# Kernel tuning notes

Hardware: AMD Instinct MI355X
Metric: run time of the kernel (lower is better)

Reference implementation:

```python
import jax, jax.numpy as jnp
import numpy as np

H = 16        # num_attention_heads
D = 1024      # hidden_size
HD = D // H   # attention_head_size = 64

def setup_inputs() -> dict:
    key = jax.random.key(0)
    ks = jax.random.split(key, 5)
    scale = 0.02
    return {
        "hidden_states": jax.random.normal(ks[0], (4, 2048, D), dtype=jnp.float32),
        "attention_mask": jnp.zeros((4, 2048), dtype=jnp.float32),
        "Wq": jax.random.normal(ks[1], (D, D), dtype=jnp.float32) * scale,
        "bq": jnp.zeros((D,), dtype=jnp.float32),
        "Wk": jax.random.normal(ks[2], (D, D), dtype=jnp.float32) * scale,
        "bk": jnp.zeros((D,), dtype=jnp.float32),
        "Wv": jax.random.normal(ks[3], (D, D), dtype=jnp.float32) * scale,
        "bv": jnp.zeros((D,), dtype=jnp.float32),
    }

def _heads(x, B, S):
    # [B,S,D] -> [B,H,S,HD]
    return x.reshape(B, S, H, HD).transpose(0, 2, 1, 3)

def reference(hidden_states, attention_mask, Wq, bq, Wk, bk, Wv, bv):
    B, S, _ = hidden_states.shape
    q = _heads(hidden_states @ Wq + bq, B, S)
    k = _heads(hidden_states @ Wk + bk, B, S)
    v = _heads(hidden_states @ Wv + bv, B, S)
    # scores: [B,H,S,S]
    scores = jnp.einsum('bhqd,bhkd->bhqk', q, k) / jnp.sqrt(jnp.float32(HD))
    scores = scores + attention_mask[:, None, None, :]  # additive mask
    probs = jax.nn.softmax(scores, axis=-1)
    # dropout is identity in eval mode
    ctx = jnp.einsum('bhqk,bhkd->bhqd', probs, v)
    return ctx.transpose(0, 2, 1, 3).reshape(B, S, H * HD)
```

## Files before the change

kernel.cpp:

```cpp
#include <hip/hip_runtime.h>


typedef __bf16 bf16_t;
typedef __bf16 bf16x2 __attribute__((ext_vector_type(2)));
typedef __bf16 bf16x4 __attribute__((ext_vector_type(4)));
typedef __bf16 bf16x8 __attribute__((ext_vector_type(8)));
typedef float floatx16 __attribute__((ext_vector_type(16)));
typedef float floatx4 __attribute__((ext_vector_type(4)));
typedef float floatx2 __attribute__((ext_vector_type(2)));

__device__ __forceinline__ void glds16(const void* g, void* l) {
  __builtin_amdgcn_global_load_lds(
      (const __attribute__((address_space(1))) void*)g,
      (__attribute__((address_space(3))) void*)l, 16, 0, 0);
}

__device__ __forceinline__ float exp2_fast(float x) {
  return __builtin_amdgcn_exp2f(x);
}

__device__ __forceinline__ unsigned pk2(float a, float b) {
  union { bf16x2 v; unsigned u; } cv;
  cv.v[0] = (bf16_t)a; cv.v[1] = (bf16_t)b;
  return cv.u;
}

__device__ __forceinline__ void plane32(unsigned& a, unsigned& b) {
  asm("v_permlane32_swap_b32 %0, %1" : "+v"(a), "+v"(b));
}

__global__ __launch_bounds__(256) void k_prep(const float* __restrict__ X,
                                              bf16_t* __restrict__ Xb,
                                              const float* __restrict__ Wq,
                                              const float* __restrict__ Wk,
                                              const float* __restrict__ Wv,
                                              bf16_t* __restrict__ Wt) {
  int bid = blockIdx.x;
  if (bid < 8192) {
    int i = (bid * 256 + threadIdx.x) * 4;
    float4 v = *(const float4*)(X + i);
    bf16x4 o;
    o[0] = (bf16_t)v.x; o[1] = (bf16_t)v.y; o[2] = (bf16_t)v.z; o[3] = (bf16_t)v.w;
    *(bf16x4*)(Xb + i) = o;
  } else {
    int t = bid - 8192;
    int z = t >> 10, r2 = t & 1023;
    int bx = r2 & 31, by = r2 >> 5;
    const float* W = (z == 0) ? Wq : ((z == 1) ? Wk : Wv);
    bf16_t* dst = Wt + (size_t)z * 1048576;
    __shared__ float tt[32][33];
    int tx = threadIdx.x & 31, ty = threadIdx.x >> 5;
#pragma unroll
    for (int r = 0; r < 4; r++) {
      int k = by * 32 + ty + r * 8;
      tt[ty + r * 8][tx] = W[k * 1024 + bx * 32 + tx];
    }
    __syncthreads();
#pragma unroll
    for (int r = 0; r < 4; r++) {
      int n = bx * 32 + ty + r * 8;
      dst[(size_t)n * 1024 + by * 32 + tx] = (bf16_t)tt[tx][ty + r * 8];
    }
  }
}

#define QKV_STAGE(kt, slot)                                   \
  do {                                                        \
    bf16_t* sA_ = lds + (slot) * 24576;                       \
    bf16_t* sB_ = sA_ + 8192;                                 \
    glds16(gA0 + (kt) * 64, sA_ + dA0);                       \
    glds16(gA1 + (kt) * 64, sA_ + dA1);                       \
    glds16(gB0 + (kt) * 64, sB_ + dB0);                       \
    glds16(gB1 + (kt) * 64, sB_ + dB1);                       \
    glds16(gB2 + (kt) * 64, sB_ + dB2);                       \
    glds16(gB3 + (kt) * 64, sB_ + dB3);                       \
  } while (0)

__global__ __launch_bounds__(512, 2) void k_qkv(
    const bf16_t* __restrict__ Xb, const bf16_t* __restrict__ Wt,
    const float* __restrict__ bq, const float* __restrict__ bk,
    const float* __restrict__ bv, bf16_t* __restrict__ Qb,
    bf16_t* __restrict__ Kb, bf16_t* __restrict__ Vt) {
  extern __shared__ bf16_t lds[];
  int tid = threadIdx.x, wv = tid >> 6, lane = tid & 63;
  int wvv = wv & 3, half = wv >> 2;
  int quad = lane >> 4, l16 = lane & 15;
  int wm = wvv >> 1, wn = wvv & 1;

  int id = blockIdx.x;
  int x = id & 7, w = id >> 3;
  int bn = w >> 3, pm = w & 7;
  int bm = x * 8 + pm;
  size_t m0 = (size_t)bm * 128, n0 = (size_t)bn * 256;
  int wsel = bn >> 2;

  const bf16_t* Ab = Xb + m0 * 1024;
  const bf16_t* Bb = Wt + n0 * 1024;

  const bf16_t *gA0, *gA1, *gB0, *gB1, *gB2, *gB3;
  int dA0, dA1, dB0, dB1, dB2, dB3;
  {
    int r8 = lane >> 3, l8 = lane & 7;
    int jA0 = wv * 2, jA1 = wv * 2 + 1;
    int rA0 = jA0 * 8 + r8, rA1 = jA1 * 8 + r8;
    gA0 = Ab + (size_t)rA0 * 1024 + ((l8 ^ (rA0 & 7)) * 8);
    gA1 = Ab + (size_t)rA1 * 1024 + ((l8 ^ (rA1 & 7)) * 8);
    dA0 = jA0 * 512; dA1 = jA1 * 512;
    int jB = wv * 4;
    int rB0 = (jB + 0) * 8 + r8, rB1 = (jB + 1) * 8 + r8;
    int rB2 = (jB + 2) * 8 + r8, rB3 = (jB + 3) * 8 + r8;
    gB0 = Bb + (size_t)rB0 * 1024 + ((l8 ^ (rB0 & 7)) * 8);
    gB1 = Bb + (size_t)rB1 * 1024 + ((l8 ^ (rB1 & 7)) * 8);
    gB2 = Bb + (size_t)rB2 * 1024 + ((l8 ^ (rB2 & 7)) * 8);
    gB3 = Bb + (size_t)rB3 * 1024 + ((l8 ^ (rB3 & 7)) * 8);
    dB0 = (jB + 0) * 512; dB1 = (jB + 1) * 512;
    dB2 = (jB + 2) * 512; dB3 = (jB + 3) * 512;
  }

  int ofsA[2][4], ofsB[2][4];
#pragma unroll
  for (int s = 0; s < 2; s++)
#pragma unroll
    for (int rt = 0; rt < 4; rt++) {
      int rowa = wm * 64 + rt * 16 + l16;
      ofsA[s][rt] = rowa * 64 + (((4 * s + quad) ^ (rowa & 7)) * 8);
      int rowb = wn * 64 + rt * 16 + l16;
      ofsB[s][rt] = rowb * 64 + (((4 * s + quad) ^ (rowb & 7)) * 8);
    }

  floatx4 acc[4][4];
#pragma unroll
  for (int a = 0; a < 4; a++)
#pragma unroll
    for (int b = 0; b < 4; b++)
#pragma unroll
      for (int r = 0; r < 4; r++) acc[a][b][r] = 0.f;

  QKV_STAGE(0, 0);
  QKV_STAGE(1, 1);

#pragma unroll
  for (int t = 0; t < 16; ++t) {
    asm volatile("" ::: "memory");
    __builtin_amdgcn_s_barrier();
    asm volatile("" ::: "memory");
    if (t + 2 < 16) QKV_STAGE(t + 2, (t + 2) % 3);
    if (t < 14)       asm volatile("s_waitcnt vmcnt(12)" ::: "memory");
    else if (t == 14) asm volatile("s_waitcnt vmcnt(6)" ::: "memory");
    else              asm volatile("s_waitcnt vmcnt(0)" ::: "memory");
    __builtin_amdgcn_sched_barrier(0);
    __builtin_amdgcn_s_barrier();
    asm volatile("" ::: "memory");

    const bf16_t* sA = lds + (t % 3) * 24576;
    const bf16_t* sBh = sA + 8192 + half * 8192;
    const bf16_t* fA = (wsel == 2) ? sBh : sA;
    const bf16_t* fB = (wsel == 2) ? sA : sBh;
#pragma unroll
    for (int s = 0; s < 2; s++) {
      bf16x8 av[4], bw[4];
#pragma unroll
      for (int rt = 0; rt < 4; rt++) {
        av[rt] = *(const bf16x8*)(fA + ofsA[s][rt]);
        bw[rt] = *(const bf16x8*)(fB + ofsB[s][rt]);
      }
#pragma unroll
      for (int rt = 0; rt < 4; rt++)
#pragma unroll
        for (int ct = 0; ct < 4; ct++)
          acc[rt][ct] = __builtin_amdgcn_mfma_f32_16x16x32_bf16(av[rt], bw[ct],
                                                               acc[rt][ct], 0, 0, 0);
    }
  }

  __syncthreads();
  bf16_t* shC = lds + half * 16384;
  int s0 = (int)(m0 & 2047), bb = (int)(m0 >> 11);
  int n0h = (int)(n0 & 1023) + half * 128;
  int hbase = n0h >> 6;
  int th = tid & 255;

  if (wsel == 2) {
#pragma unroll
    for (int rt = 0; rt < 4; rt++) {
#pragma unroll
      for (int r = 0; r < 4; r++) {
        int nl = wm * 64 + rt * 16 + quad * 4 + r;
        float bi = bv[n0h + nl];
#pragma unroll
        for (int ct = 0; ct < 4; ct++) {
          int ml = wn * 64 + ct * 16 + l16;
          shC[nl * 128 + ml] = (bf16_t)(acc[rt][ct][r] + bi);
        }
      }
    }
    __syncthreads();
#pragma unroll
    for (int p = 0; p < 8; p++) {
      int c = p * 256 + th;
      int nl = c >> 4, mo = (c & 15) * 8;
      bf16x8 vv = *(const bf16x8*)(shC + nl * 128 + mo);
      int hh = hbase + (nl >> 6), dd = nl & 63;
      *(bf16x8*)(Vt + (size_t)(bb * 16 + hh) * 131072 + (size_t)dd * 2048 + s0 + mo) = vv;
    }
  } else {
    const float* bias = (wsel == 0) ? bq : bk;
#pragma unroll
    for (int ct = 0; ct < 4; ct++) {
      int nl = wn * 64 + ct * 16 + l16;
      float bi = bias[n0h + nl];
#pragma unroll
      for (int rt = 0; rt < 4; rt++) {
#pragma unroll
        for (int r = 0; r < 4; r++) {
          int ml = wm * 64 + rt * 16 + quad * 4 + r;
          float v = acc[rt][ct][r] + bi;
          shC[ml * 128 + nl] =
              (wsel == 0) ? (bf16_t)(v * 0.18033688011117f) : (bf16_t)v;
        }
      }
    }
    __syncthreads();
    bf16_t* outp = (wsel == 0) ? Qb : Kb;
#pragma unroll
    for (int p = 0; p < 8; p++) {
      int c = p * 256 + th;
      int h = c >> 10, c1 = c & 1023;
      int ml = c1 >> 3, ko = (c1 & 7) * 8;
      bf16x8 vv = *(const bf16x8*)(shC + ml * 128 + h * 64 + ko);
      *(bf16x8*)(outp + (size_t)(bb * 16 + hbase + h) * 131072 +
                 (size_t)(s0 + ml) * 64 + ko) = vv;
    }
  }
}

__global__ __launch_bounds__(256, 2) void k_attn(const bf16_t* __restrict__ Qb,
                                                 const bf16_t* __restrict__ Kb,
                                                 const bf16_t* __restrict__ VtG,
                                                 const float* __restrict__ mask,
                                                 float* __restrict__ out) {
  __shared__ float smem[10240];
  bf16_t* lds = (bf16_t*)smem;
  float* mlds = smem + 8192;

  int tid = threadIdx.x, wq = tid >> 6, lane = tid & 63;
  int q5 = lane & 31, h5 = lane >> 5;

  int id = blockIdx.x;
  int x = id & 7, w = id >> 3;
  int bh = x * 8 + (w >> 3), qt = w & 7;
  int b = bh >> 4, hh = bh & 15;

  const bf16_t* Qp = Qb + (size_t)bh * 131072;
  const bf16_t* Kp = Kb + (size_t)bh * 131072;
  const bf16_t* Vp = VtG + (size_t)bh * 131072;
  const float* mp = mask + b * 2048;

#pragma unroll
  for (int j = 0; j < 2; j++) {
    float4 mv = *(const float4*)(mp + tid * 8 + j * 4);
    float4 sv;
    sv.x = mv.x * 1.4426950408890f - 12.0f;
    sv.y = mv.y * 1.4426950408890f - 12.0f;
    sv.z = mv.z * 1.4426950408890f - 12.0f;
    sv.w = mv.w * 1.4426950408890f - 12.0f;
    *(float4*)(mlds + tid * 8 + j * 4) = sv;
  }

  int q0 = qt * 256 + wq * 64;
  bf16x8 qf0[4], qf1[4];
#pragma unroll
  for (int s = 0; s < 4; s++) {
    qf0[s] = *(const bf16x8*)(Qp + (size_t)(q0 + q5) * 64 + s * 16 + h5 * 8);
    qf1[s] = *(const bf16x8*)(Qp + (size_t)(q0 + 32 + q5) * 64 + s * 16 + h5 * 8);
  }

  union { uint4 u; bf16x8 v; } qfe;
  qfe.u.x = h5 ? 0u : 0x00003f80u;
  qfe.u.y = 0u; qfe.u.z = 0u; qfe.u.w = 0u;

  int off[2][4];
#pragma unroll
  for (int j = 0; j < 2; j++)
#pragma unroll
    for (int s = 0; s < 4; s++)
      off[j][s] = (j * 32 + q5) * 64 + (((2 * s + h5) ^ (q5 & 7)) * 8);

  int r0 = wq * 16 + (lane >> 3);
  int slot = (lane & 7) ^ ((lane >> 3) & 7);
  const bf16_t* kg0 = Kp + (size_t)r0 * 64 + slot * 8;
  const bf16_t* kg1 = kg0 + 512;
  const bf16_t* vg0 = Vp + (size_t)r0 * 2048 + slot * 8;
  const bf16_t* vg1 = vg0 + 16384;
  int c0 = wq * 2;

  floatx16 zed;
#pragma unroll
  for (int r = 0; r < 16; r++) zed[r] = 0.f;

  floatx16 ov[4];
#pragma unroll
  for (int t2 = 0; t2 < 4; t2++)
#pragma unroll
    for (int r = 0; r < 16; r++) ov[t2][r] = 0.f;
  floatx2 pA0, pA1, pB0, pB1;
  pA0[0] = pA0[1] = pA1[0] = pA1[1] = 0.f;
  pB0[0] = pB0[1] = pB1[0] = pB1[1] = 0.f;

  {
    bf16_t* bK = lds;
    bf16_t* bV = lds + 4096;
    glds16(kg0, bK + c0 * 512); glds16(kg1, bK + c0 * 512 + 512);
    glds16(vg0, bV + c0 * 512); glds16(vg1, bV + c0 * 512 + 512);
    kg0 += 4096; kg1 += 4096; vg0 += 64; vg1 += 64;
  }

  for (int it = 0; it < 32; ++it) {
    int kk0 = it * 64, cur = it & 1;
    __syncthreads();
    if (it + 1 < 32) {
      bf16_t* bK = lds + (cur ^ 1) * 8192;
      bf16_t* bV = bK + 4096;
      glds16(kg0, bK + c0 * 512); glds16(kg1, bK + c0 * 512 + 512);
      glds16(vg0, bV + c0 * 512); glds16(vg1, bV + c0 * 512 + 512);
      kg0 += 4096; kg1 += 4096; vg0 += 64; vg1 += 64;
    }
    const bf16_t* bK = lds + cur * 8192;
    const bf16_t* bV = bK + 4096;

    union { uint4 u; bf16x8 v; } kfe[2];
    kfe[0].u.x = h5 ? 0u : pk2(mlds[kk0 + q5], 0.f);
    kfe[1].u.x = h5 ? 0u : pk2(mlds[kk0 + 32 + q5], 0.f);
    kfe[0].u.y = 0u; kfe[0].u.z = 0u; kfe[0].u.w = 0u;
    kfe[1].u.y = 0u; kfe[1].u.z = 0u; kfe[1].u.w = 0u;

#pragma unroll
    for (int tt = 0; tt < 2; tt++) {
      bf16x8 kf[4], vfa[2], vfb[2];
#pragma unroll
      for (int s = 0; s < 4; s++) kf[s] = *(const bf16x8*)(bK + off[tt][s]);
#pragma unroll
      for (int t2 = 0; t2 < 2; t2++) {
        vfa[t2] = *(const bf16x8*)(bV + off[t2][tt * 2]);
        vfb[t2] = *(const bf16x8*)(bV + off[t2][tt * 2 + 1]);
      }

      floatx16 a0, a1;
      __builtin_amdgcn_s_setprio(1);
      floatx16 mt = __builtin_amdgcn_mfma_f32_32x32x16_bf16(kfe[tt].v, qfe.v, zed, 0, 0, 0);
      a0 = __builtin_amdgcn_mfma_f32_32x32x16_bf16(kf[0], qf0[0], mt, 0, 0, 0);
      a1 = __builtin_amdgcn_mfma_f32_32x32x16_bf16(kf[0], qf1[0], mt, 0, 0, 0);
#pragma unroll
      for (int s = 1; s < 4; s++) {
        a0 = __builtin_amdgcn_mfma_f32_32x32x16_bf16(kf[s], qf0[s], a0, 0, 0, 0);
        a1 = __builtin_amdgcn_mfma_f32_32x32x16_bf16(kf[s], qf1[s], a1, 0, 0, 0);
      }
      __builtin_amdgcn_s_setprio(0);

#pragma unroll
      for (int sl = 0; sl < 2; sl++) {
        int base = sl * 8;
        float e0 = exp2_fast(a0[base + 0]);
        float e1 = exp2_fast(a0[base + 1]);
        float e2 = exp2_fast(a0[base + 2]);
        float e3 = exp2_fast(a0[base + 3]);
        float e4 = exp2_fast(a0[base + 4]);
        float e5 = exp2_fast(a0[base + 5]);
        float e6 = exp2_fast(a0[base + 6]);
        float e7 = exp2_fast(a0[base + 7]);
        floatx2 u0, u1;
        u0[0] = e0 + e4; u0[1] = e1 + e5; pA0 += u0;
        u1[0] = e2 + e6; u1[1] = e3 + e7; pA1 += u1;
        unsigned A0 = pk2(e0, e1), B0 = pk2(e2, e3);
        unsigned C0 = pk2(e4, e5), D0 = pk2(e6, e7);
        float f0 = exp2_fast(a1[base + 0]);
        float f1 = exp2_fast(a1[base + 1]);
        float f2 = exp2_fast(a1[base + 2]);
        float f3 = exp2_fast(a1[base + 3]);
        float f4 = exp2_fast(a1[base + 4]);
        float f5 = exp2_fast(a1[base + 5]);
        float f6 = exp2_fast(a1[base + 6]);
        float f7 = exp2_fast(a1[base + 7]);
        floatx2 w0, w1;
        w0[0] = f0 + f4; w0[1] = f1 + f5; pB0 += w0;
        w1[0] = f2 + f6; w1[1] = f3 + f7; pB1 += w1;
        unsigned A1 = pk2(f0, f1), B1 = pk2(f2, f3);
        unsigned C1 = pk2(f4, f5), D1 = pk2(f6, f7);
        unsigned px0 = A0, pz0 = C0; plane32(px0, pz0);
        unsigned py0 = B0, pw0 = D0; plane32(py0, pw0);
        unsigned px1 = A1, pz1 = C1; plane32(px1, pz1);
        unsigned py1 = B1, pw1 = D1; plane32(py1, pw1);
        union { uint4 u; bf16x8 v; } pf0, pf1;
        pf0.u.x = px0; pf0.u.y = py0; pf0.u.z = pz0; pf0.u.w = pw0;
        pf1.u.x = px1; pf1.u.y = py1; pf1.u.z = pz1; pf1.u.w = pw1;
        __builtin_amdgcn_s_setprio(1);
#pragma unroll
        for (int t2 = 0; t2 < 2; t2++) {
          bf16x8 vf = sl ? vfb[t2] : vfa[t2];
          ov[t2]     = __builtin_amdgcn_mfma_f32_32x32x16_bf16(vf, pf0.v, ov[t2], 0, 0, 0);
          ov[2 + t2] = __builtin_amdgcn_mfma_f32_32x32x16_bf16(vf, pf1.v, ov[2 + t2], 0, 0, 0);
        }
        __builtin_amdgcn_s_setprio(0);
      }
    }
  }

  float ls0 = (pA0[0] + pA0[1]) + (pA1[0] + pA1[1]);
  float ls1 = (pB0[0] + pB0[1]) + (pB1[0] + pB1[1]);
  ls0 += __shfl_xor(ls0, 32);
  ls1 += __shfl_xor(ls1, 32);
  float rl0 = 1.f / ls0, rl1 = 1.f / ls1;

  int qbase0 = b * 2048 + qt * 256;
#pragma unroll
  for (int half = 0; half < 2; half++) {
    __syncthreads();
    if ((wq >> 1) == half) {
      int qw = (wq & 1) * 64;
#pragma unroll
      for (int u = 0; u < 2; u++) {
        float rl = u ? rl1 : rl0;
#pragma unroll
        for (int t2 = 0; t2 < 2; t2++)
#pragma unroll
          for (int r = 0; r < 16; r++) {
            int d = t2 * 32 + (r & 3) + 8 * (r >> 2) + 4 * h5;
            smem[(qw + u * 32 + q5) * 68 + d] = ov[u * 2 + t2][r] * rl;
          }
      }
    }
    __syncthreads();
    int qbase = qbase0 + half * 128;
#pragma unroll
    for (int i = 0; i < 8; i++) {
      int slot2 = i * 256 + tid;
      int q = slot2 >> 4, c = slot2 & 15;
      float4 v = *(const float4*)(smem + q * 68 + c * 4);
      *(float4*)(out + (size_t)(qbase + q) * 1024 + hh * 64 + c * 4) = v;
    }
  }
}

extern "C" void kernel_launch(void* const* d_in, const int* in_sizes, int n_in,
                              void* d_out, int out_size, void* d_ws, size_t ws_size,
                              hipStream_t stream) {
  const float* X    = (const float*)d_in[0];
  const float* mask = (const float*)d_in[1];
  const float* Wq   = (const float*)d_in[2];
  const float* bq   = (const float*)d_in[3];
  const float* Wk   = (const float*)d_in[4];
  const float* bk   = (const float*)d_in[5];
  const float* Wv   = (const float*)d_in[6];
  const float* bv   = (const float*)d_in[7];
  float* out = (float*)d_out;

  char* ws = (char*)d_ws;
  bf16_t* Xb = (bf16_t*)ws;
  bf16_t* Wt = (bf16_t*)(ws + 16777216);
  bf16_t* Qb = (bf16_t*)(ws + 23068672);
  bf16_t* Kb = (bf16_t*)(ws + 39845888);
  bf16_t* Vt = (bf16_t*)(ws + 56623104);

  k_prep<<<11264, 256, 0, stream>>>(X, Xb, Wq, Wk, Wv, Wt);
  k_qkv<<<768, 512, 147456, stream>>>(Xb, Wt, bq, bk, bv, Qb, Kb, Vt);
  k_attn<<<512, 256, 0, stream>>>(Qb, Kb, Vt, mask, out);
}
```

Measured before the change: 233.1 us.

## Split QKV GEMM prefetch into halves interleaved with MFMA sub-steps

The per-stage global-to-LDS prefetch in the QKV projection GEMM is split into two halves. Each half is issued just before one of the two k-substeps of MFMA work, with an extra barrier between the substeps and adjusted vmcnt waits. MFMA sections are wrapped in s_setprio to favor math issue. The aim is to spread memory issue across compute and reduce stalls at the stage boundary, at the cost of an additional workgroup barrier per iteration.

```diff
diff --git a/kernel.cpp b/kernel.cpp
--- a/kernel.cpp
+++ b/kernel.cpp
@@ -64,13 +64,18 @@
   }
 }
 
-#define QKV_STAGE(kt, slot)                                   \
+#define QKV_STAGE_A(kt, slot)                                 \
   do {                                                        \
     bf16_t* sA_ = lds + (slot) * 24576;                       \
     bf16_t* sB_ = sA_ + 8192;                                 \
     glds16(gA0 + (kt) * 64, sA_ + dA0);                       \
     glds16(gA1 + (kt) * 64, sA_ + dA1);                       \
     glds16(gB0 + (kt) * 64, sB_ + dB0);                       \
+  } while (0)
+#define QKV_STAGE_B(kt, slot)                                 \
+  do {                                                        \
+    bf16_t* sA_ = lds + (slot) * 24576;                       \
+    bf16_t* sB_ = sA_ + 8192;                                 \
     glds16(gB1 + (kt) * 64, sB_ + dB1);                       \
     glds16(gB2 + (kt) * 64, sB_ + dB2);                       \
     glds16(gB3 + (kt) * 64, sB_ + dB3);                       \
@@ -136,18 +141,15 @@
 #pragma unroll
       for (int r = 0; r < 4; r++) acc[a][b][r] = 0.f;
 
-  QKV_STAGE(0, 0);
-  QKV_STAGE(1, 1);
+  QKV_STAGE_A(0, 0); QKV_STAGE_B(0, 0);
+  QKV_STAGE_A(1, 1); QKV_STAGE_B(1, 1);
 
 #pragma unroll
   for (int t = 0; t < 16; ++t) {
     asm volatile("" ::: "memory");
     __builtin_amdgcn_s_barrier();
-    asm volatile("" ::: "memory");
-    if (t + 2 < 16) QKV_STAGE(t + 2, (t + 2) % 3);
-    if (t < 14)       asm volatile("s_waitcnt vmcnt(12)" ::: "memory");
-    else if (t == 14) asm volatile("s_waitcnt vmcnt(6)" ::: "memory");
-    else              asm volatile("s_waitcnt vmcnt(0)" ::: "memory");
+    if (t < 15) asm volatile("s_waitcnt vmcnt(6)" ::: "memory");
+    else        asm volatile("s_waitcnt vmcnt(0)" ::: "memory");
     __builtin_amdgcn_sched_barrier(0);
     __builtin_amdgcn_s_barrier();
     asm volatile("" ::: "memory");
@@ -156,20 +158,44 @@
     const bf16_t* sBh = sA + 8192 + half * 8192;
     const bf16_t* fA = (wsel == 2) ? sBh : sA;
     const bf16_t* fB = (wsel == 2) ? sA : sBh;
-#pragma unroll
-    for (int s = 0; s < 2; s++) {
+
+    if (t + 2 < 16) QKV_STAGE_A(t + 2, (t + 2) % 3);
+    {
       bf16x8 av[4], bw[4];
 #pragma unroll
       for (int rt = 0; rt < 4; rt++) {
-        av[rt] = *(const bf16x8*)(fA + ofsA[s][rt]);
-        bw[rt] = *(const bf16x8*)(fB + ofsB[s][rt]);
-      }
+        av[rt] = *(const bf16x8*)(fA + ofsA[0][rt]);
+        bw[rt] = *(const bf16x8*)(fB + ofsB[0][rt]);
+      }
+      __builtin_amdgcn_s_setprio(1);
 #pragma unroll
       for (int rt = 0; rt < 4; rt++)
 #pragma unroll
         for (int ct = 0; ct < 4; ct++)
           acc[rt][ct] = __builtin_amdgcn_mfma_f32_16x16x32_bf16(av[rt], bw[ct],
                                                                acc[rt][ct], 0, 0, 0);
+      __builtin_amdgcn_s_setprio(0);
+    }
+    asm volatile("" ::: "memory");
+    __builtin_amdgcn_s_barrier();
+    asm volatile("" ::: "memory");
+
+    if (t + 2 < 16) QKV_STAGE_B(t + 2, (t + 2) % 3);
+    {
+      bf16x8 av[4], bw[4];
+#pragma unroll
+      for (int rt = 0; rt < 4; rt++) {
+        av[rt] = *(const bf16x8*)(fA + ofsA[1][rt]);
+        bw[rt] = *(const bf16x8*)(fB + ofsB[1][rt]);
+      }
+      __builtin_amdgcn_s_setprio(1);
+#pragma unroll
+      for (int rt = 0; rt < 4; rt++)
+#pragma unroll
+        for (int ct = 0; ct < 4; ct++)
+          acc[rt][ct] = __builtin_amdgcn_mfma_f32_16x16x32_bf16(av[rt], bw[ct],
+                                                               acc[rt][ct], 0, 0, 0);
+      __builtin_amdgcn_s_setprio(0);
     }
   }
 
```

After: 224.5 us. 3.7% less time.
